# Kernel optimization log

Measured on AMD Instinct MI355X. Metric: run time of the kernel, lower is better.

## Reference

```python
import jax, jax.numpy as jnp
import numpy as np

V, N, K, D = 100000, 20000, 32, 128
NEG = -1e9  # masked logit value


def setup_inputs() -> dict:
    key = jax.random.key(0)
    ks = jax.random.split(key, 8)
    return {
        "nodes": jax.random.randint(ks[0], (N,), 0, V),
        "neigh_idx": jax.random.randint(ks[1], (N, K), 0, V),
        "degrees": jax.random.randint(ks[2], (N,), 0, K + 1),
        "u2e": jax.random.normal(ks[3], (V, D), dtype=jnp.float32),
        "W1": jax.random.normal(ks[4], (2 * D, D), dtype=jnp.float32) * 0.05,
        "b1": jnp.zeros((D,), jnp.float32),
        "W2": jax.random.normal(ks[5], (D, D), dtype=jnp.float32) * 0.05,
        "b2": jnp.zeros((D,), jnp.float32),
        "W3": jax.random.normal(ks[6], (D, 1), dtype=jnp.float32) * 0.05,
        "b3": jnp.zeros((1,), jnp.float32),
    }


def reference(nodes, neigh_idx, degrees, u2e, W1, b1, W2, b2, W3, b3):
    self_feats = u2e[nodes]                      # [N, D]
    e_u = u2e[neigh_idx]                         # [N, K, D] ragged gather (padded)
    # Attention MLP: cat(neighbor, self) -> relu -> relu -> scalar logit
    x = jnp.concatenate([e_u, jnp.broadcast_to(self_feats[:, None, :], (e_u.shape[0], K, D))], axis=-1)  # [N, K, 2D]
    h = jax.nn.relu(x @ W1 + b1)                 # [N, K, D]
    h = jax.nn.relu(h @ W2 + b2)                 # [N, K, D]
    logits = (h @ W3 + b3)[..., 0]               # [N, K]
    mask = jnp.arange(K)[None, :] < degrees[:, None]
    att = jax.nn.softmax(jnp.where(mask, logits, NEG), axis=-1)  # softmax over neighbors
    agg = jnp.einsum("nk,nkd->nd", att, e_u)     # attention-weighted neighbor sum
    out = jnp.where(degrees[:, None] > 0, (agg + self_feats) * 0.5, self_feats)
    return out
```

## Files before the change

### kernel.cpp

```cpp
#include <hip/hip_runtime.h>
#include <hip/hip_bf16.h>

#define KK 32
#define DD 128
#define NEGV (-1e9f)
#define SE 136

typedef __attribute__((ext_vector_type(8))) short bf16x8;
typedef __attribute__((ext_vector_type(8))) unsigned short u16x8;
typedef __attribute__((ext_vector_type(4))) float f32x4;

__device__ __forceinline__ unsigned short f2bf(float f) {
    union { float f; unsigned u; } v; v.f = f;
    unsigned r = v.u + 0x7fffu + ((v.u >> 16) & 1u);
    return (unsigned short)(r >> 16);
}
__device__ __forceinline__ float bf2f(unsigned short h) {
    union { unsigned u; float f; } v; v.u = ((unsigned)h) << 16;
    return v.f;
}
__device__ __forceinline__ unsigned pk2(float x, float y) {
    union { __hip_bfloat162 h; unsigned u; } c;
    c.h = __float22bfloat162_rn(float2{x, y});
    return c.u;
}

__global__ __launch_bounds__(256) void prep_kernel(const float* __restrict__ W1,
                                                   const float* __restrict__ W2,
                                                   unsigned short* __restrict__ W1t,
                                                   unsigned short* __restrict__ W2t) {
    const int id = blockIdx.x * 256 + threadIdx.x;
    if (id < 256 * 128) {
        const int n = id >> 8, k = id & 255;
        W1t[id] = f2bf(W1[k * DD + n]);
    } else {
        const int j = id - 256 * 128;
        const int n = j >> 7, k = j & 127;
        W2t[j] = f2bf(W2[k * DD + n]);
    }
}

__global__ __launch_bounds__(256, 2) void ppagg_mfma(
    const int* __restrict__ nodes, const int* __restrict__ neigh,
    const int* __restrict__ degrees, const float* __restrict__ u2e,
    const unsigned short* __restrict__ W1t, const unsigned short* __restrict__ W2t,
    const float* __restrict__ b1, const float* __restrict__ b2,
    const float* __restrict__ W3, const float* __restrict__ b3,
    float* __restrict__ out, const int Nn)
{
    __shared__ __align__(16) unsigned short s_eh[128 * SE];
    __shared__ __align__(16) unsigned short s_x[4 * DD];
    __shared__ __align__(16) float s_xf[4 * DD];
    __shared__ float s_w3[DD];
    __shared__ float s_att[128];
    __shared__ int   s_idx[128];

    const int tid  = threadIdx.x;
    const int w    = tid >> 6;
    const int lane = tid & 63;
    const int ln   = lane & 15;
    const int q    = lane >> 4;

    if (tid < DD) s_w3[tid] = W3[tid];

    bf16x8 b1f[8][2], b2f[4][2];
    float b1c[2], b2c[2];
    #pragma unroll
    for (int nt = 0; nt < 2; ++nt) {
        const int c = w * 32 + nt * 16 + ln;
        #pragma unroll
        for (int kk = 0; kk < 8; ++kk)
            b1f[kk][nt] = *(const bf16x8*)(W1t + c * 256 + kk * 32 + q * 8);
        #pragma unroll
        for (int kk = 0; kk < 4; ++kk)
            b2f[kk][nt] = *(const bf16x8*)(W2t + c * 128 + kk * 32 + q * 8);
        b1c[nt] = b1[c];
        b2c[nt] = b2[c];
    }

    const int nodes_base = blockIdx.x * 8;

    for (int it = 0; it < 2; ++it) {
        const int gbase = nodes_base + it * 4;

        {
            const int r = tid & 127;
            const int h = tid >> 7;
            int ng = gbase + (r >> 5);
            if (ng >= Nn) ng = Nn - 1;
            const int idx = neigh[ng * KK + (r & 31)];
            if (h == 0) s_idx[r] = idx;
            const float4* src = (const float4*)(u2e + (long)idx * DD + h * 64);
            unsigned short* dst = s_eh + r * SE + h * 64;
            #pragma unroll
            for (int c8 = 0; c8 < 8; ++c8) {
                const float4 v0 = src[c8 * 2];
                const float4 v1 = src[c8 * 2 + 1];
                uint4 p;
                p.x = pk2(v0.x, v0.y); p.y = pk2(v0.z, v0.w);
                p.z = pk2(v1.x, v1.y); p.w = pk2(v1.z, v1.w);
                *(uint4*)(dst + c8 * 8) = p;
            }
            int ngs = gbase + w;
            if (ngs >= Nn) ngs = Nn - 1;
            const int snode = nodes[ngs];
            const float2 sv = *(const float2*)(u2e + (long)snode * DD + lane * 2);
            *(float2*)(s_xf + w * DD + lane * 2) = sv;
            *(unsigned*)(s_x + w * DD + lane * 2) = pk2(sv.x, sv.y);
        }
        __syncthreads();

        f32x4 acc[8][2];
        #pragma unroll
        for (int mt = 0; mt < 8; ++mt) {
            acc[mt][0] = (f32x4){0.f, 0.f, 0.f, 0.f};
            acc[mt][1] = (f32x4){0.f, 0.f, 0.f, 0.f};
        }
        #pragma unroll
        for (int kk = 0; kk < 4; ++kk) {
            bf16x8 a[8];
            #pragma unroll
            for (int mt = 0; mt < 8; ++mt)
                a[mt] = *(const bf16x8*)(s_eh + (mt * 16 + ln) * SE + kk * 32 + q * 8);
            #pragma unroll
            for (int mt = 0; mt < 8; ++mt) {
                acc[mt][0] = __builtin_amdgcn_mfma_f32_16x16x32_bf16(a[mt], b1f[kk][0], acc[mt][0], 0, 0, 0);
                acc[mt][1] = __builtin_amdgcn_mfma_f32_16x16x32_bf16(a[mt], b1f[kk][1], acc[mt][1], 0, 0, 0);
            }
        }
        #pragma unroll
        for (int kk = 4; kk < 8; ++kk) {
            #pragma unroll
            for (int mt = 0; mt < 8; ++mt) {
                const bf16x8 a = *(const bf16x8*)(s_x + (mt >> 1) * DD + (kk - 4) * 32 + q * 8);
                acc[mt][0] = __builtin_amdgcn_mfma_f32_16x16x32_bf16(a, b1f[kk][0], acc[mt][0], 0, 0, 0);
                acc[mt][1] = __builtin_amdgcn_mfma_f32_16x16x32_bf16(a, b1f[kk][1], acc[mt][1], 0, 0, 0);
            }
        }
        __syncthreads();

        #pragma unroll
        for (int mt = 0; mt < 8; ++mt)
            #pragma unroll
            for (int nt = 0; nt < 2; ++nt) {
                const int c = w * 32 + nt * 16 + ln;
                #pragma unroll
                for (int r = 0; r < 4; ++r) {
                    const int row = mt * 16 + q * 4 + r;
                    s_eh[row * SE + c] = f2bf(fmaxf(acc[mt][nt][r] + b1c[nt], 0.f));
                }
            }
        __syncthreads();

        f32x4 acc2[8][2];
        #pragma unroll
        for (int mt = 0; mt < 8; ++mt) {
            acc2[mt][0] = (f32x4){0.f, 0.f, 0.f, 0.f};
            acc2[mt][1] = (f32x4){0.f, 0.f, 0.f, 0.f};
        }
        #pragma unroll
        for (int kk = 0; kk < 4; ++kk) {
            bf16x8 a[8];
            #pragma unroll
            for (int mt = 0; mt < 8; ++mt)
                a[mt] = *(const bf16x8*)(s_eh + (mt * 16 + ln) * SE + kk * 32 + q * 8);
            #pragma unroll
            for (int mt = 0; mt < 8; ++mt) {
                acc2[mt][0] = __builtin_amdgcn_mfma_f32_16x16x32_bf16(a[mt], b2f[kk][0], acc2[mt][0], 0, 0, 0);
                acc2[mt][1] = __builtin_amdgcn_mfma_f32_16x16x32_bf16(a[mt], b2f[kk][1], acc2[mt][1], 0, 0, 0);
            }
        }
        __syncthreads();

        #pragma unroll
        for (int mt = 0; mt < 8; ++mt)
            #pragma unroll
            for (int nt = 0; nt < 2; ++nt) {
                const int c = w * 32 + nt * 16 + ln;
                #pragma unroll
                for (int r = 0; r < 4; ++r) {
                    const int row = mt * 16 + q * 4 + r;
                    s_eh[row * SE + c] = f2bf(fmaxf(acc2[mt][nt][r] + b2c[nt], 0.f));
                }
            }
        __syncthreads();

        if (tid < 128) {
            const int row = tid;
            const unsigned short* hp = s_eh + row * SE;
            float dot = 0.f;
            #pragma unroll
            for (int c8 = 0; c8 < 16; ++c8) {
                const u16x8 hv = *(const u16x8*)(hp + c8 * 8);
                #pragma unroll
                for (int j = 0; j < 8; ++j)
                    dot = fmaf(bf2f(hv[j]), s_w3[c8 * 8 + j], dot);
            }
            const float logit = dot + b3[0];
            int ng = gbase + (row >> 5);
            if (ng >= Nn) ng = Nn - 1;
            const int deg = degrees[ng];
            const float ml = ((row & 31) < deg) ? logit : NEGV;
            float mx = ml;
            #pragma unroll
            for (int off = 16; off > 0; off >>= 1) mx = fmaxf(mx, __shfl_xor(mx, off));
            const float e = __expf(ml - mx);
            float ssum = e;
            #pragma unroll
            for (int off = 16; off > 0; off >>= 1) ssum += __shfl_xor(ssum, off);
            s_att[row] = e / ssum;
        }
        __syncthreads();

        {
            const int ng = gbase + w;
            const int d0 = lane * 2;
            float ax = 0.f, ay = 0.f;
            #pragma unroll 8
            for (int k = 0; k < KK; ++k) {
                const int   ridx = s_idx[w * KK + k];
                const float a    = s_att[w * KK + k];
                const float2 ev  = *(const float2*)(u2e + (long)ridx * DD + d0);
                ax = fmaf(a, ev.x, ax);
                ay = fmaf(a, ev.y, ay);
            }
            if (ng < Nn) {
                const int deg = degrees[ng];
                const float sx = s_xf[w * DD + d0];
                const float sy = s_xf[w * DD + d0 + 1];
                float2 o;
                o.x = (deg > 0) ? 0.5f * (ax + sx) : sx;
                o.y = (deg > 0) ? 0.5f * (ay + sy) : sy;
                *(float2*)(out + (long)ng * DD + d0) = o;
            }
        }
        __syncthreads();
    }
}

extern "C" void kernel_launch(void* const* d_in, const int* in_sizes, int n_in,
                              void* d_out, int out_size, void* d_ws, size_t ws_size,
                              hipStream_t stream) {
    const int*   nodes   = (const int*)d_in[0];
    const int*   neigh   = (const int*)d_in[1];
    const int*   degrees = (const int*)d_in[2];
    const float* u2e     = (const float*)d_in[3];
    const float* W1      = (const float*)d_in[4];
    const float* b1      = (const float*)d_in[5];
    const float* W2      = (const float*)d_in[6];
    const float* b2      = (const float*)d_in[7];
    const float* W3      = (const float*)d_in[8];
    const float* b3      = (const float*)d_in[9];
    float* out = (float*)d_out;

    unsigned short* W1t = (unsigned short*)d_ws;
    unsigned short* W2t = W1t + 256 * 128;

    const int Nn = in_sizes[0];

    prep_kernel<<<192, 256, 0, stream>>>(W1, W2, W1t, W2t);
    const int grid = (Nn + 7) / 8;
    ppagg_mfma<<<grid, 256, 0, stream>>>(nodes, neigh, degrees, u2e,
                                         W1t, W2t, b1, b2, W3, b3, out, Nn);
}
```

Before: 235.8 us.

## Reuse staged bf16 neighbor rows for aggregation instead of re-gathering from global

Before layer-1 results overwrite shared memory, each wave copies its node's bf16 neighbor embeddings into 32 registers. The final weighted sum then reads those registers instead of gathering fp32 rows from u2e a second time. Self features stay in registers, the s_idx and s_xf shared arrays are removed, the ReLU outputs are packed two at a time, and launch bounds target 3 blocks per SM. This removes a second random global gather, but the aggregation now uses bf16-rounded embeddings, which lowers accuracy. It also adds register pressure and one extra barrier.

```diff
diff --git a/kernel.cpp b/kernel.cpp
--- a/kernel.cpp
+++ b/kernel.cpp
@@ -40,7 +40,7 @@
     }
 }
 
-__global__ __launch_bounds__(256, 2) void ppagg_mfma(
+__global__ __launch_bounds__(256, 3) void ppagg_mfma(
     const int* __restrict__ nodes, const int* __restrict__ neigh,
     const int* __restrict__ degrees, const float* __restrict__ u2e,
     const unsigned short* __restrict__ W1t, const unsigned short* __restrict__ W2t,
@@ -50,10 +50,8 @@
 {
     __shared__ __align__(16) unsigned short s_eh[128 * SE];
     __shared__ __align__(16) unsigned short s_x[4 * DD];
-    __shared__ __align__(16) float s_xf[4 * DD];
     __shared__ float s_w3[DD];
     __shared__ float s_att[128];
-    __shared__ int   s_idx[128];
 
     const int tid  = threadIdx.x;
     const int w    = tid >> 6;
@@ -83,13 +81,13 @@
     for (int it = 0; it < 2; ++it) {
         const int gbase = nodes_base + it * 4;
 
+        float2 selfv;
         {
             const int r = tid & 127;
             const int h = tid >> 7;
             int ng = gbase + (r >> 5);
             if (ng >= Nn) ng = Nn - 1;
             const int idx = neigh[ng * KK + (r & 31)];
-            if (h == 0) s_idx[r] = idx;
             const float4* src = (const float4*)(u2e + (long)idx * DD + h * 64);
             unsigned short* dst = s_eh + r * SE + h * 64;
             #pragma unroll
@@ -104,9 +102,8 @@
             int ngs = gbase + w;
             if (ngs >= Nn) ngs = Nn - 1;
             const int snode = nodes[ngs];
-            const float2 sv = *(const float2*)(u2e + (long)snode * DD + lane * 2);
-            *(float2*)(s_xf + w * DD + lane * 2) = sv;
-            *(unsigned*)(s_x + w * DD + lane * 2) = pk2(sv.x, sv.y);
+            selfv = *(const float2*)(u2e + (long)snode * DD + lane * 2);
+            *(unsigned*)(s_x + w * DD + lane * 2) = pk2(selfv.x, selfv.y);
         }
         __syncthreads();
 
@@ -139,15 +136,24 @@
         }
         __syncthreads();
 
+        unsigned pe[KK];
+        #pragma unroll
+        for (int k = 0; k < KK; ++k)
+            pe[k] = *(const unsigned*)(s_eh + (w * KK + k) * SE + (lane << 1));
+        __syncthreads();
+
         #pragma unroll
         for (int mt = 0; mt < 8; ++mt)
             #pragma unroll
             for (int nt = 0; nt < 2; ++nt) {
                 const int c = w * 32 + nt * 16 + ln;
                 #pragma unroll
-                for (int r = 0; r < 4; ++r) {
+                for (int r = 0; r < 4; r += 2) {
+                    const unsigned p = pk2(fmaxf(acc[mt][nt][r]     + b1c[nt], 0.f),
+                                           fmaxf(acc[mt][nt][r + 1] + b1c[nt], 0.f));
                     const int row = mt * 16 + q * 4 + r;
-                    s_eh[row * SE + c] = f2bf(fmaxf(acc[mt][nt][r] + b1c[nt], 0.f));
+                    s_eh[row * SE + c]       = (unsigned short)(p & 0xffffu);
+                    s_eh[(row + 1) * SE + c] = (unsigned short)(p >> 16);
                 }
             }
         __syncthreads();
@@ -178,9 +184,12 @@
             for (int nt = 0; nt < 2; ++nt) {
                 const int c = w * 32 + nt * 16 + ln;
                 #pragma unroll
-                for (int r = 0; r < 4; ++r) {
+                for (int r = 0; r < 4; r += 2) {
+                    const unsigned p = pk2(fmaxf(acc2[mt][nt][r]     + b2c[nt], 0.f),
+                                           fmaxf(acc2[mt][nt][r + 1] + b2c[nt], 0.f));
                     const int row = mt * 16 + q * 4 + r;
-                    s_eh[row * SE + c] = f2bf(fmaxf(acc2[mt][nt][r] + b2c[nt], 0.f));
+                    s_eh[row * SE + c]       = (unsigned short)(p & 0xffffu);
+                    s_eh[(row + 1) * SE + c] = (unsigned short)(p >> 16);
                 }
             }
         __syncthreads();
@@ -214,24 +223,21 @@
 
         {
             const int ng = gbase + w;
-            const int d0 = lane * 2;
             float ax = 0.f, ay = 0.f;
-            #pragma unroll 8
+            #pragma unroll
             for (int k = 0; k < KK; ++k) {
-                const int   ridx = s_idx[w * KK + k];
-                const float a    = s_att[w * KK + k];
-                const float2 ev  = *(const float2*)(u2e + (long)ridx * DD + d0);
-                ax = fmaf(a, ev.x, ax);
-                ay = fmaf(a, ev.y, ay);
+                const float a  = s_att[w * KK + k];
+                const float lo = bf2f((unsigned short)(pe[k] & 0xffffu));
+                const float hi = bf2f((unsigned short)(pe[k] >> 16));
+                ax = fmaf(a, lo, ax);
+                ay = fmaf(a, hi, ay);
             }
             if (ng < Nn) {
                 const int deg = degrees[ng];
-                const float sx = s_xf[w * DD + d0];
-                const float sy = s_xf[w * DD + d0 + 1];
                 float2 o;
-                o.x = (deg > 0) ? 0.5f * (ax + sx) : sx;
-                o.y = (deg > 0) ? 0.5f * (ay + sy) : sy;
-                *(float2*)(out + (long)ng * DD + d0) = o;
+                o.x = (deg > 0) ? 0.5f * (ax + selfv.x) : selfv.x;
+                o.y = (deg > 0) ? 0.5f * (ay + selfv.y) : selfv.y;
+                *(float2*)(out + (long)ng * DD + lane * 2) = o;
             }
         }
         __syncthreads();
```

New measurement: 332.4 us. +41.0%, slower.
